# Performance work log

Measured on AMD Instinct MI355X. Metric: run time of the kernel, lower is better.

## Reference

```python
import jax, jax.numpy as jnp
import numpy as np

DIM = 192
NUM_TOKENS = 64
RD = 10
B, N = 32, 4096
EPS = 1e-12  # F.normalize eps


def setup_inputs() -> dict:
    key = jax.random.key(0)
    ks = jax.random.split(key, 9)
    s = 1.0 / np.sqrt(DIM)
    return {
        "x": jax.random.normal(ks[0], (B, N, DIM), dtype=jnp.float32),
        "td": jax.random.normal(ks[1], (B, NUM_TOKENS, DIM), dtype=jnp.float32),
        "wq_w": jax.random.uniform(ks[2], (RD, DIM), jnp.float32, -s, s),
        "wq_b": jax.random.uniform(ks[3], (RD,), jnp.float32, -s, s),
        "wk_w": jax.random.uniform(ks[4], (RD, DIM), jnp.float32, -s, s),
        "wk_b": jax.random.uniform(ks[5], (RD,), jnp.float32, -s, s),
        "wv_w": jax.random.uniform(ks[6], (DIM, DIM), jnp.float32, -s, s),
        "wv_b": jax.random.uniform(ks[7], (DIM,), jnp.float32, -s, s),
        "scale": jnp.ones((1,), dtype=jnp.float32),
        "x_size": 64,
    }


def _l2norm(t):
    # matches F.normalize(dim=-1, eps=1e-12): x / max(||x||, eps)
    n = jnp.sqrt(jnp.sum(t * t, axis=-1, keepdims=True))
    return t / jnp.maximum(n, EPS)


def reference(x, td, wq_w, wq_b, wk_w, wk_b, wv_w, wv_b, scale, x_size):
    # q: (b, n, dr); k: (b, m, dr); v: (b, m, c)
    q = jnp.einsum("bnc,dc->bnd", x, wq_w) + wq_b
    k = jnp.einsum("bmc,dc->bmd", td, wk_w) + wk_b
    v = jnp.einsum("bmc,ec->bme", td, wv_w) + wv_b
    # cosine similarity attention logits: (b, n, m)
    attn = jnp.einsum("bnd,bmd->bnm", _l2norm(q), _l2norm(k))
    attn = attn * (1.0 + jnp.clip(scale, 0.0, 3.0) * np.log(NUM_TOKENS))
    attn = jax.nn.softmax(attn, axis=-1)
    out = jnp.einsum("bnm,bme->bne", attn, v)  # (b, n, c)
    return out, attn
```

## Files before the change

### kernel.cpp

```cpp
#include <hip/hip_runtime.h>
#include <math.h>

#define DIM 192
#define NT 64
#define RD 10
#define BB 32
#define NN 4096
#define LN64 4.1588830833596715f

typedef __attribute__((ext_vector_type(8))) short short8v;
typedef __attribute__((ext_vector_type(4))) float float4v;

#define WQF_OFF 0
#define KNF_OFF 4096
#define VF_OFF  (4096 + 32 * 2048)

__device__ __forceinline__ ushort f2bf(float f) {
    union { float f; unsigned u; } v; v.f = f;
    unsigned r = (v.u + 0x7fffu + ((v.u >> 16) & 1u)) >> 16;
    return (ushort)r;
}
__device__ __forceinline__ float bf2f(ushort h) {
    union { unsigned u; float f; } v; v.u = ((unsigned)h) << 16;
    return v.f;
}

__global__ __launch_bounds__(256, 2) void ATD_prep(
        const float* __restrict__ td,
        const float* __restrict__ wk_w, const float* __restrict__ wk_b,
        const float* __restrict__ wv_w, const float* __restrict__ wv_b,
        const float* __restrict__ wq_w,
        ushort* __restrict__ wsu) {
    __shared__ float smem[15696];
    const int b = blockIdx.x, y = blockIdx.y, t = threadIdx.x;
    const float* tdb = td + (size_t)b * NT * DIM;

    if (y < 12) {
        float4* td_s = (float4*)smem;
        float4* wv_s = (float4*)(smem + 64 * 196);
        float*  wvb_s = smem + 64 * 196 + 16 * 196;

        const float4* tds = (const float4*)tdb;
        #pragma unroll
        for (int j = 0; j < 12; ++j) {
            int idx = t + 256 * j;
            td_s[(idx / 48) * 49 + (idx % 48)] = tds[idx];
        }
        const float4* wvs = (const float4*)(wv_w + (size_t)(y * 16) * DIM);
        #pragma unroll
        for (int j = 0; j < 3; ++j) {
            int idx = t + 256 * j;
            wv_s[(idx / 48) * 49 + (idx % 48)] = wvs[idx];
        }
        if (t < 16) wvb_s[t] = wv_b[y * 16 + t];
        __syncthreads();

        const int ks = t >> 7;
        const int l  = (t >> 1) & 63;
        const int ih = t & 1;
        const int mb = ks * 32 + (l >> 4) * 8 + ih * 4;
        const int e  = l & 15;

        float a0 = wvb_s[e], a1 = a0, a2 = a0, a3 = a0;
        const float4* w4 = wv_s + e * 49;
        const float4* t0 = td_s + (mb + 0) * 49;
        const float4* t1 = td_s + (mb + 1) * 49;
        const float4* t2 = td_s + (mb + 2) * 49;
        const float4* t3 = td_s + (mb + 3) * 49;
        #pragma unroll 4
        for (int c4 = 0; c4 < 48; ++c4) {
            float4 w = w4[c4];
            float4 r0 = t0[c4], r1 = t1[c4], r2 = t2[c4], r3 = t3[c4];
            a0 += r0.x * w.x + r0.y * w.y + r0.z * w.z + r0.w * w.w;
            a1 += r1.x * w.x + r1.y * w.y + r1.z * w.z + r1.w * w.w;
            a2 += r2.x * w.x + r2.y * w.y + r2.z * w.z + r2.w * w.w;
            a3 += r3.x * w.x + r3.y * w.y + r3.z * w.z + r3.w * w.w;
        }
        ushort o[4] = {f2bf(a0), f2bf(a1), f2bf(a2), f2bf(a3)};
        *(uint2*)(wsu + VF_OFF + (size_t)b * 12288 + ks * 6144 + y * 512 + l * 8 + ih * 4)
            = *(uint2*)o;
    } else {
        float* kp   = smem;
        float* kn_s = smem + 3072;

        const int m = t & 63, ch = t >> 6;
        float k[RD];
        #pragma unroll
        for (int d = 0; d < RD; ++d) k[d] = 0.f;
        const float4* td4 = (const float4*)(tdb + (size_t)m * DIM) + ch * 12;
        #pragma unroll 4
        for (int c4 = 0; c4 < 12; ++c4) {
            float4 a = td4[c4];
            #pragma unroll
            for (int d = 0; d < RD; ++d) {
                float4 w = ((const float4*)(wk_w + (size_t)d * DIM))[ch * 12 + c4];
                k[d] += a.x * w.x + a.y * w.y + a.z * w.z + a.w * w.w;
            }
        }
        #pragma unroll
        for (int d = 0; d < RD; ++d) kp[(ch * 64 + m) * 12 + d] = k[d];
        __syncthreads();
        if (t < NT) {
            float kk[RD], ss = 0.f;
            #pragma unroll
            for (int d = 0; d < RD; ++d) {
                kk[d] = wk_b[d] + kp[t * 12 + d] + kp[(64 + t) * 12 + d]
                      + kp[(128 + t) * 12 + d] + kp[(192 + t) * 12 + d];
                ss += kk[d] * kk[d];
            }
            float rn = 1.f / fmaxf(sqrtf(ss), 1e-12f);
            #pragma unroll
            for (int d = 0; d < 16; ++d)
                kn_s[t * 16 + d] = (d < RD) ? kk[d] * rn : 0.f;
        }
        __syncthreads();
        {
            int mt = t >> 6, l = t & 63;
            ushort tmp[8];
            #pragma unroll
            for (int i = 0; i < 8; ++i) {
                int d = (l >> 4) * 8 + i;
                int mm = mt * 16 + (l & 15);
                tmp[i] = (d < 16) ? f2bf(kn_s[mm * 16 + d]) : (ushort)0;
            }
            *(uint4*)(wsu + KNF_OFF + (size_t)b * 2048 + t * 8) = *(uint4*)tmp;
        }
        if (b == 0) {
            for (int s = t; s < 384; s += 256) {
                int ksq = s >> 6, l = s & 63;
                ushort tmp[8];
                #pragma unroll
                for (int i = 0; i < 8; ++i) {
                    int d = l & 15;
                    int c = ksq * 32 + (l >> 4) * 8 + i;
                    tmp[i] = (d < RD) ? f2bf(wq_w[(size_t)d * DIM + c]) : (ushort)0;
                }
                *(uint4*)(wsu + WQF_OFF + s * 8) = *(uint4*)tmp;
            }
        }
    }
}

__global__ __launch_bounds__(256, 3) void ATD_main(
        const float* __restrict__ x, const float* __restrict__ wq_b,
        const float* __restrict__ scale, const ushort* __restrict__ wsu,
        float* __restrict__ out, float* __restrict__ attn) {
    __shared__ ushort p_lds[256 * 64];
    __shared__ ushort qn_lds[4][512];

    const int t = threadIdx.x, w = t >> 6, l = t & 63;
    const int b = blockIdx.y;
    const int rb0 = blockIdx.x * 256;

    ((unsigned*)qn_lds)[t]       = 0u;
    ((unsigned*)qn_lds)[t + 256] = 0u;
    ((unsigned*)qn_lds)[t + 512] = 0u;
    ((unsigned*)qn_lds)[t + 768] = 0u;

    short8v wqf[6], knf[4];
    #pragma unroll
    for (int ks = 0; ks < 6; ++ks)
        wqf[ks] = *(const short8v*)(wsu + WQF_OFF + ks * 512 + l * 8);
    #pragma unroll
    for (int mt = 0; mt < 4; ++mt)
        knf[mt] = *(const short8v*)(wsu + KNF_OFF + (size_t)b * 2048 + mt * 512 + l * 8);

    const float bias = ((l & 15) < RD) ? wq_b[l & 15] : 0.f;
    const float factor = 1.0f + fminf(fmaxf(scale[0], 0.f), 3.f) * LN64;

    __syncthreads();

    char* qnbase = (char*)(&qn_lds[w][0]);
    const float4v z4 = {0.f, 0.f, 0.f, 0.f};

    #pragma unroll 1
    for (int rt = 0; rt < 4; ++rt) {
        const int rbase = rb0 + w * 64 + rt * 16;

        float4v qacc = {bias, bias, bias, bias};
        const float* xr = x + ((size_t)b * NN + rbase + (l & 15)) * DIM + (l >> 4) * 8;
        #pragma unroll
        for (int ks = 0; ks < 6; ++ks) {
            float4 f0 = *(const float4*)(xr + ks * 32);
            float4 f1 = *(const float4*)(xr + ks * 32 + 4);
            float xv[8] = {f0.x, f0.y, f0.z, f0.w, f1.x, f1.y, f1.z, f1.w};
            short8v xhi, xlo;
            #pragma unroll
            for (int i = 0; i < 8; ++i) {
                ushort h = f2bf(xv[i]);
                xhi[i] = (short)h;
                xlo[i] = (short)f2bf(xv[i] - bf2f(h));
            }
            qacc = __builtin_amdgcn_mfma_f32_16x16x32_bf16(xhi, wqf[ks], qacc, 0, 0, 0);
            qacc = __builtin_amdgcn_mfma_f32_16x16x32_bf16(xlo, wqf[ks], qacc, 0, 0, 0);
        }

        float sj[4];
        #pragma unroll
        for (int j = 0; j < 4; ++j) sj[j] = qacc[j] * qacc[j];
        #pragma unroll
        for (int mm = 1; mm < 16; mm <<= 1) {
            #pragma unroll
            for (int j = 0; j < 4; ++j) sj[j] += __shfl_xor(sj[j], mm, 64);
        }
        #pragma unroll
        for (int j = 0; j < 4; ++j) {
            float rn = 1.f / fmaxf(sqrtf(sj[j]), 1e-12f);
            int row = (l >> 4) * 4 + j, col = l & 15;
            int addr = row * 64 + ((col * 2) ^ ((row & 3) << 4));
            *(ushort*)(qnbase + addr) = f2bf(qacc[j] * rn);
        }

        int arow = l & 15;
        int aaddr = arow * 64 + ((((l >> 4) * 16)) ^ ((arow & 3) << 4));
        short8v qnA = *(short8v*)(qnbase + aaddr);
        float4v sA[4];
        #pragma unroll
        for (int mt = 0; mt < 4; ++mt)
            sA[mt] = __builtin_amdgcn_mfma_f32_16x16x32_bf16(qnA, knf[mt], z4, 0, 0, 0);

        float mx[4], sum[4], pv[4][4];
        #pragma unroll
        for (int j = 0; j < 4; ++j)
            mx[j] = fmaxf(fmaxf(sA[0][j], sA[1][j]), fmaxf(sA[2][j], sA[3][j]));
        #pragma unroll
        for (int mm = 1; mm < 16; mm <<= 1) {
            #pragma unroll
            for (int j = 0; j < 4; ++j) mx[j] = fmaxf(mx[j], __shfl_xor(mx[j], mm, 64));
        }
        #pragma unroll
        for (int j = 0; j < 4; ++j) sum[j] = 0.f;
        #pragma unroll
        for (int mt = 0; mt < 4; ++mt) {
            #pragma unroll
            for (int j = 0; j < 4; ++j) {
                float e = __expf((sA[mt][j] - mx[j]) * factor);
                pv[mt][j] = e; sum[j] += e;
            }
        }
        #pragma unroll
        for (int mm = 1; mm < 16; mm <<= 1) {
            #pragma unroll
            for (int j = 0; j < 4; ++j) sum[j] += __shfl_xor(sum[j], mm, 64);
        }
        #pragma unroll
        for (int j = 0; j < 4; ++j) sum[j] = 1.f / sum[j];
        #pragma unroll
        for (int mt = 0; mt < 4; ++mt)
            #pragma unroll
            for (int j = 0; j < 4; ++j) pv[mt][j] *= sum[j];

        float* ab = attn + ((size_t)b * NN + rbase) * NT;
        #pragma unroll
        for (int mt = 0; mt < 4; ++mt)
            #pragma unroll
            for (int j = 0; j < 4; ++j)
                ab[((l >> 4) * 4 + j) * NT + (l & 15) + 16 * mt] = pv[mt][j];

        #pragma unroll
        for (int mt = 0; mt < 4; ++mt)
            #pragma unroll
            for (int j = 0; j < 4; ++j) {
                int row = w * 64 + rt * 16 + (l >> 4) * 4 + j;
                int m = (l & 15) + 16 * mt;
                int addr = row * 128 + ((m * 2) ^ ((row & 7) << 4));
                *(ushort*)((char*)p_lds + addr) = f2bf(pv[mt][j]);
            }
    }
    __syncthreads();

    const ushort* vfb = wsu + VF_OFF + (size_t)b * 12288;
    #pragma unroll 1
    for (int ct = 0; ct < 12; ++ct) {
        short8v B0 = *(const short8v*)(vfb + ct * 512 + l * 8);
        short8v B1 = *(const short8v*)(vfb + 6144 + ct * 512 + l * 8);
        #pragma unroll
        for (int rt = 0; rt < 4; ++rt) {
            int rloc = w * 64 + rt * 16 + (l & 15);
            int a0 = rloc * 128 + ((((l >> 4) * 16)) ^ ((rloc & 7) << 4));
            int a1 = rloc * 128 + ((64 + ((l >> 4) * 16)) ^ ((rloc & 7) << 4));
            short8v A0 = *(short8v*)((char*)p_lds + a0);
            short8v A1 = *(short8v*)((char*)p_lds + a1);
            float4v acc = __builtin_amdgcn_mfma_f32_16x16x32_bf16(A0, B0, z4, 0, 0, 0);
            acc = __builtin_amdgcn_mfma_f32_16x16x32_bf16(A1, B1, acc, 0, 0, 0);
            float* ob = out + ((size_t)b * NN + rb0 + w * 64 + rt * 16) * DIM + ct * 16 + (l & 15);
            #pragma unroll
            for (int j = 0; j < 4; ++j)
                ob[((l >> 4) * 4 + j) * DIM] = acc[j];
        }
    }
}

extern "C" void kernel_launch(void* const* d_in, const int* in_sizes, int n_in,
                              void* d_out, int out_size, void* d_ws, size_t ws_size,
                              hipStream_t stream) {
    const float* x     = (const float*)d_in[0];
    const float* td    = (const float*)d_in[1];
    const float* wq_w  = (const float*)d_in[2];
    const float* wq_b  = (const float*)d_in[3];
    const float* wk_w  = (const float*)d_in[4];
    const float* wk_b  = (const float*)d_in[5];
    const float* wv_w  = (const float*)d_in[6];
    const float* wv_b  = (const float*)d_in[7];
    const float* scale = (const float*)d_in[8];

    float* out  = (float*)d_out;
    float* attn = out + (size_t)BB * NN * DIM;
    ushort* wsu = (ushort*)d_ws;

    ATD_prep<<<dim3(BB, 13), 256, 0, stream>>>(td, wk_w, wk_b, wv_w, wv_b, wq_w, wsu);
    ATD_main<<<dim3(NN / 256, BB), 256, 0, stream>>>(x, wq_b, scale, wsu, out, attn);
}
```

Before: 63.91 us.

## Fuse softmax and PV per wave tile, drop block barriers, halve rows per block

```diff
diff --git a/kernel.cpp b/kernel.cpp
--- a/kernel.cpp
+++ b/kernel.cpp
@@ -19,10 +19,6 @@
     union { float f; unsigned u; } v; v.f = f;
     unsigned r = (v.u + 0x7fffu + ((v.u >> 16) & 1u)) >> 16;
     return (ushort)r;
-}
-__device__ __forceinline__ float bf2f(ushort h) {
-    union { unsigned u; float f; } v; v.u = ((unsigned)h) << 16;
-    return v.f;
 }
 
 __global__ __launch_bounds__(256, 2) void ATD_prep(
@@ -141,21 +137,24 @@
     }
 }
 
-__global__ __launch_bounds__(256, 3) void ATD_main(
+__global__ __launch_bounds__(256, 4) void ATD_main(
         const float* __restrict__ x, const float* __restrict__ wq_b,
         const float* __restrict__ scale, const ushort* __restrict__ wsu,
         float* __restrict__ out, float* __restrict__ attn) {
-    __shared__ ushort p_lds[256 * 64];
-    __shared__ ushort qn_lds[4][512];
+    __shared__ ushort qn_lds[4][16 * 32];
+    __shared__ ushort p_lds[4][16 * 64];
 
     const int t = threadIdx.x, w = t >> 6, l = t & 63;
     const int b = blockIdx.y;
-    const int rb0 = blockIdx.x * 256;
-
-    ((unsigned*)qn_lds)[t]       = 0u;
-    ((unsigned*)qn_lds)[t + 256] = 0u;
-    ((unsigned*)qn_lds)[t + 512] = 0u;
-    ((unsigned*)qn_lds)[t + 768] = 0u;
+    const int rb0 = blockIdx.x * 128;
+    const int lg = l >> 4;
+    const int lc = l & 15;
+
+    {
+        unsigned* z = (unsigned*)(&qn_lds[w][0]);
+        #pragma unroll
+        for (int i = 0; i < 4; ++i) z[l + 64 * i] = 0u;
+    }
 
     short8v wqf[6], knf[4];
     #pragma unroll
@@ -165,32 +164,39 @@
     for (int mt = 0; mt < 4; ++mt)
         knf[mt] = *(const short8v*)(wsu + KNF_OFF + (size_t)b * 2048 + mt * 512 + l * 8);
 
-    const float bias = ((l & 15) < RD) ? wq_b[l & 15] : 0.f;
+    const float bias = (lc < RD) ? wq_b[lc] : 0.f;
     const float factor = 1.0f + fminf(fmaxf(scale[0], 0.f), 3.f) * LN64;
 
-    __syncthreads();
-
     char* qnbase = (char*)(&qn_lds[w][0]);
+    char* pbase  = (char*)(&p_lds[w][0]);
     const float4v z4 = {0.f, 0.f, 0.f, 0.f};
+    const ushort* vfb = wsu + VF_OFF + (size_t)b * 12288;
 
     #pragma unroll 1
-    for (int rt = 0; rt < 4; ++rt) {
-        const int rbase = rb0 + w * 64 + rt * 16;
+    for (int rt = 0; rt < 2; ++rt) {
+        const int rbase = rb0 + w * 32 + rt * 16;
 
         float4v qacc = {bias, bias, bias, bias};
-        const float* xr = x + ((size_t)b * NN + rbase + (l & 15)) * DIM + (l >> 4) * 8;
+        const float* xr = x + ((size_t)b * NN + rbase + lc) * DIM + lg * 8;
         #pragma unroll
         for (int ks = 0; ks < 6; ++ks) {
             float4 f0 = *(const float4*)(xr + ks * 32);
             float4 f1 = *(const float4*)(xr + ks * 32 + 4);
             float xv[8] = {f0.x, f0.y, f0.z, f0.w, f1.x, f1.y, f1.z, f1.w};
-            short8v xhi, xlo;
-            #pragma unroll
-            for (int i = 0; i < 8; ++i) {
-                ushort h = f2bf(xv[i]);
-                xhi[i] = (short)h;
-                xlo[i] = (short)f2bf(xv[i] - bf2f(h));
-            }
+            unsigned hi[4], lo[4];
+            #pragma unroll
+            for (int i = 0; i < 4; ++i) {
+                unsigned a = __float_as_uint(xv[2 * i]);
+                unsigned c = __float_as_uint(xv[2 * i + 1]);
+                hi[i] = (a >> 16) | (c & 0xFFFF0000u);
+                float h0 = __uint_as_float(a & 0xFFFF0000u);
+                float h1 = __uint_as_float(c & 0xFFFF0000u);
+                float d0 = xv[2 * i] - h0;
+                float d1 = xv[2 * i + 1] - h1;
+                lo[i] = (__float_as_uint(d0) >> 16) | (__float_as_uint(d1) & 0xFFFF0000u);
+            }
+            short8v xhi = *(short8v*)hi;
+            short8v xlo = *(short8v*)lo;
             qacc = __builtin_amdgcn_mfma_f32_16x16x32_bf16(xhi, wqf[ks], qacc, 0, 0, 0);
             qacc = __builtin_amdgcn_mfma_f32_16x16x32_bf16(xlo, wqf[ks], qacc, 0, 0, 0);
         }
@@ -206,87 +212,87 @@
         #pragma unroll
         for (int j = 0; j < 4; ++j) {
             float rn = 1.f / fmaxf(sqrtf(sj[j]), 1e-12f);
-            int row = (l >> 4) * 4 + j, col = l & 15;
-            int addr = row * 64 + ((col * 2) ^ ((row & 3) << 4));
+            int row = lg * 4 + j;
+            int addr = (row * 64 + lc * 2) ^ (((row >> 2) & 3) << 5);
             *(ushort*)(qnbase + addr) = f2bf(qacc[j] * rn);
         }
 
-        int arow = l & 15;
-        int aaddr = arow * 64 + ((((l >> 4) * 16)) ^ ((arow & 3) << 4));
-        short8v qnA = *(short8v*)(qnbase + aaddr);
-        float4v sA[4];
-        #pragma unroll
-        for (int mt = 0; mt < 4; ++mt)
-            sA[mt] = __builtin_amdgcn_mfma_f32_16x16x32_bf16(qnA, knf[mt], z4, 0, 0, 0);
-
-        float mx[4], sum[4], pv[4][4];
-        #pragma unroll
-        for (int j = 0; j < 4; ++j)
-            mx[j] = fmaxf(fmaxf(sA[0][j], sA[1][j]), fmaxf(sA[2][j], sA[3][j]));
-        #pragma unroll
-        for (int mm = 1; mm < 16; mm <<= 1) {
-            #pragma unroll
-            for (int j = 0; j < 4; ++j) mx[j] = fmaxf(mx[j], __shfl_xor(mx[j], mm, 64));
-        }
-        #pragma unroll
-        for (int j = 0; j < 4; ++j) sum[j] = 0.f;
-        #pragma unroll
-        for (int mt = 0; mt < 4; ++mt) {
-            #pragma unroll
-            for (int j = 0; j < 4; ++j) {
-                float e = __expf((sA[mt][j] - mx[j]) * factor);
-                pv[mt][j] = e; sum[j] += e;
-            }
-        }
-        #pragma unroll
-        for (int mm = 1; mm < 16; mm <<= 1) {
-            #pragma unroll
-            for (int j = 0; j < 4; ++j) sum[j] += __shfl_xor(sum[j], mm, 64);
-        }
-        #pragma unroll
-        for (int j = 0; j < 4; ++j) sum[j] = 1.f / sum[j];
-        #pragma unroll
-        for (int mt = 0; mt < 4; ++mt)
-            #pragma unroll
-            for (int j = 0; j < 4; ++j) pv[mt][j] *= sum[j];
-
-        float* ab = attn + ((size_t)b * NN + rbase) * NT;
-        #pragma unroll
-        for (int mt = 0; mt < 4; ++mt)
+        {
+            int arow = lc;
+            int aaddr = (arow * 64 + lg * 16) ^ (((arow >> 2) & 3) << 5);
+            short8v qnA = *(short8v*)(qnbase + aaddr);
+            float4v sA[4];
+            #pragma unroll
+            for (int mt = 0; mt < 4; ++mt)
+                sA[mt] = __builtin_amdgcn_mfma_f32_16x16x32_bf16(qnA, knf[mt], z4, 0, 0, 0);
+
+            float mx[4], sum[4], pv[4][4];
             #pragma unroll
             for (int j = 0; j < 4; ++j)
-                ab[((l >> 4) * 4 + j) * NT + (l & 15) + 16 * mt] = pv[mt][j];
-
-        #pragma unroll
-        for (int mt = 0; mt < 4; ++mt)
-            #pragma unroll
-            for (int j = 0; j < 4; ++j) {
-                int row = w * 64 + rt * 16 + (l >> 4) * 4 + j;
-                int m = (l & 15) + 16 * mt;
-                int addr = row * 128 + ((m * 2) ^ ((row & 7) << 4));
-                *(ushort*)((char*)p_lds + addr) = f2bf(pv[mt][j]);
-            }
-    }
-    __syncthreads();
-
-    const ushort* vfb = wsu + VF_OFF + (size_t)b * 12288;
-    #pragma unroll 1
-    for (int ct = 0; ct < 12; ++ct) {
-        short8v B0 = *(const short8v*)(vfb + ct * 512 + l * 8);
-        short8v B1 = *(const short8v*)(vfb + 6144 + ct * 512 + l * 8);
-        #pragma unroll
-        for (int rt = 0; rt < 4; ++rt) {
-            int rloc = w * 64 + rt * 16 + (l & 15);
-            int a0 = rloc * 128 + ((((l >> 4) * 16)) ^ ((rloc & 7) << 4));
-            int a1 = rloc * 128 + ((64 + ((l >> 4) * 16)) ^ ((rloc & 7) << 4));
-            short8v A0 = *(short8v*)((char*)p_lds + a0);
-            short8v A1 = *(short8v*)((char*)p_lds + a1);
-            float4v acc = __builtin_amdgcn_mfma_f32_16x16x32_bf16(A0, B0, z4, 0, 0, 0);
-            acc = __builtin_amdgcn_mfma_f32_16x16x32_bf16(A1, B1, acc, 0, 0, 0);
-            float* ob = out + ((size_t)b * NN + rb0 + w * 64 + rt * 16) * DIM + ct * 16 + (l & 15);
-            #pragma unroll
-            for (int j = 0; j < 4; ++j)
-                ob[((l >> 4) * 4 + j) * DIM] = acc[j];
+                mx[j] = fmaxf(fmaxf(sA[0][j], sA[1][j]), fmaxf(sA[2][j], sA[3][j]));
+            #pragma unroll
+            for (int mm = 1; mm < 16; mm <<= 1) {
+                #pragma unroll
+                for (int j = 0; j < 4; ++j) mx[j] = fmaxf(mx[j], __shfl_xor(mx[j], mm, 64));
+            }
+            #pragma unroll
+            for (int j = 0; j < 4; ++j) sum[j] = 0.f;
+            #pragma unroll
+            for (int mt = 0; mt < 4; ++mt) {
+                #pragma unroll
+                for (int j = 0; j < 4; ++j) {
+                    float e = __expf((sA[mt][j] - mx[j]) * factor);
+                    pv[mt][j] = e; sum[j] += e;
+                }
+            }
+            #pragma unroll
+            for (int mm = 1; mm < 16; mm <<= 1) {
+                #pragma unroll
+                for (int j = 0; j < 4; ++j) sum[j] += __shfl_xor(sum[j], mm, 64);
+            }
+            #pragma unroll
+            for (int j = 0; j < 4; ++j) sum[j] = 1.f / sum[j];
+            #pragma unroll
+            for (int mt = 0; mt < 4; ++mt)
+                #pragma unroll
+                for (int j = 0; j < 4; ++j) pv[mt][j] *= sum[j];
+
+            float* ab = attn + ((size_t)b * NN + rbase) * NT;
+            #pragma unroll
+            for (int mt = 0; mt < 4; ++mt)
+                #pragma unroll
+                for (int j = 0; j < 4; ++j)
+                    ab[(lg * 4 + j) * NT + lc + 16 * mt] = pv[mt][j];
+
+            #pragma unroll
+            for (int mt = 0; mt < 4; ++mt)
+                #pragma unroll
+                for (int j = 0; j < 4; ++j) {
+                    int row = lg * 4 + j;
+                    int m = lc + 16 * mt;
+                    int addr = (row * 128 + m * 2) ^ (((row >> 2) & 3) << 5);
+                    *(ushort*)(pbase + addr) = f2bf(pv[mt][j]);
+                }
+        }
+
+        {
+            int arow = lc;
+            int xorm = ((arow >> 2) & 3) << 5;
+            int a0 = (arow * 128 + lg * 16) ^ xorm;
+            int a1 = (arow * 128 + 64 + lg * 16) ^ xorm;
+            short8v A0 = *(short8v*)(pbase + a0);
+            short8v A1 = *(short8v*)(pbase + a1);
+            float* ob = out + ((size_t)b * NN + rbase) * DIM + lc;
+            #pragma unroll
+            for (int ct = 0; ct < 12; ++ct) {
+                short8v B0 = *(const short8v*)(vfb + ct * 512 + l * 8);
+                short8v B1 = *(const short8v*)(vfb + 6144 + ct * 512 + l * 8);
+                float4v acc = __builtin_amdgcn_mfma_f32_16x16x32_bf16(A0, B0, z4, 0, 0, 0);
+                acc = __builtin_amdgcn_mfma_f32_16x16x32_bf16(A1, B1, acc, 0, 0, 0);
+                #pragma unroll
+                for (int j = 0; j < 4; ++j)
+                    ob[(lg * 4 + j) * DIM + ct * 16] = acc[j];
+            }
         }
     }
 }
@@ -309,5 +315,5 @@
     ushort* wsu = (ushort*)d_ws;
 
     ATD_prep<<<dim3(BB, 13), 256, 0, stream>>>(td, wk_w, wk_b, wv_w, wv_b, wq_w, wsu);
-    ATD_main<<<dim3(NN / 256, BB), 256, 0, stream>>>(x, wq_b, scale, wsu, out, attn);
+    ATD_main<<<dim3(NN / 128, BB), 256, 0, stream>>>(x, wq_b, scale, wsu, out, attn);
 }
```

After: 109.0 us. 70.5% more time.
